# Optimization experiments

Hardware: AMD Instinct MI355X
Metric: run time of the kernel (lower is better)

## Reference

```python
import jax, jax.numpy as jnp
import numpy as np

# EISANI constants (inference path, dense non-EI weights, static connections)
NUM_BITS = 16        # EISANITABcontinuousVarEncodingNumBits
K_SYN = 32           # numberOfSynapsesPerSegment
SEGMENTS = 2         # numberOfSegmentsPerNeuron
THETA = 8            # segment activation threshold (synapse-count based)
H = 4096             # hiddenLayerSize
F = 128              # numberOfFeatures
C = 10               # numberOfClasses
B = 64               # batch


def _make_weight(key, h, s, p):
    """Dense weight [h, s, p] with exactly K_SYN nonzero +/-1 synapses per segment
    (mirrors _initialise_layer_weights dense non-EI branch)."""
    k1, k2 = jax.random.split(key)
    cols = jax.random.randint(k1, (h, s, K_SYN), 0, p)
    signs = jnp.where(jax.random.bernoulli(k2, 0.5, (h, s, K_SYN)), 1.0, -1.0).astype(jnp.float32)
    hh = jnp.arange(h)[:, None, None]
    ss = jnp.arange(s)[None, :, None]
    return jnp.zeros((h, s, p), jnp.float32).at[hh, ss, cols].set(signs)


def setup_inputs() -> dict:
    key = jax.random.key(0)
    kx, k0, k1, k2, ko = jax.random.split(key, 5)
    x = jax.random.uniform(kx, (B, F), dtype=jnp.float32)
    W0 = _make_weight(k0, H, SEGMENTS, F * NUM_BITS)
    W1 = _make_weight(k1, H, SEGMENTS, H)
    W2 = _make_weight(k2, H, SEGMENTS, H)
    outW = jax.random.normal(ko, (3, H, C), dtype=jnp.float32) * 0.02
    return {"x": x, "W0": W0, "W1": W1, "W2": W2, "outW": outW}


def _encode(x):
    # thermometer (graded) encoding of continuous vars into NUM_BITS binary bits
    thresholds = (jnp.arange(NUM_BITS, dtype=jnp.float32) + 1.0) / (NUM_BITS + 1.0)
    bits = (x[:, :, None] >= thresholds).astype(jnp.float32)  # [B, F, NUM_BITS]
    return bits.reshape(x.shape[0], -1)  # [B, F*NUM_BITS]


def reference(x, W0, W1, W2, outW):
    acts = _encode(x)  # [B, P0]
    layer_acts = []
    for W in (W0, W1, W2):
        # segment membrane sums over binary presynaptic activations
        z = jnp.einsum('bp,hsp->bhs', acts, W)  # [B, H, S]
        # neuron fires if ANY segment reaches threshold
        fired = jnp.any(z >= THETA, axis=-1)
        acts = fired.astype(jnp.float32)  # binary activation [B, H]
        layer_acts.append(acts)
    stacked = jnp.stack(layer_acts)  # [L, B, H]
    out = jnp.einsum('lbh,lhc->bc', stacked, outW)  # class scores [B, C]
    return out
```

## Files before the change

kernel.cpp:

```cpp
#include <hip/hip_runtime.h>
#include <hip/hip_bf16.h>

typedef unsigned long long u64;
typedef float f32x4 __attribute__((ext_vector_type(4)));

#define H_SZ 4096
#define NBITS 16
#define NFEAT 128
#define NCLS 10
#define THETA 8


__global__ void encode_kernel(const float* __restrict__ x, u64* __restrict__ actp0) {
    int idx = blockIdx.x * blockDim.x + threadIdx.x;
    if (idx >= 32 * 64) return;
    int wword = idx >> 6;
    int b = idx & 63;
    int c = wword >> 2, j = wword & 3;
    float thr0 = (4 * 0 + j + 1.0f) / (NBITS + 1.0f);
    float thr1 = (4 * 1 + j + 1.0f) / (NBITS + 1.0f);
    float thr2 = (4 * 2 + j + 1.0f) / (NBITS + 1.0f);
    float thr3 = (4 * 3 + j + 1.0f) / (NBITS + 1.0f);
    const float* xb = x + b * NFEAT + c * 16;
    u64 word = 0;
    #pragma unroll
    for (int k = 0; k < 16; k++) {
        float xv = xb[k];
        word |= (u64)(xv >= thr0) << (4 * k + 0);
        word |= (u64)(xv >= thr1) << (4 * k + 1);
        word |= (u64)(xv >= thr2) << (4 * k + 2);
        word |= (u64)(xv >= thr3) << (4 * k + 3);
    }
    actp0[wword * 64 + b] = word;
}

__device__ __forceinline__ u64 bfly_stage(u64 x, int lane, int d, u64 Md) {
    u64 p = __shfl_xor(x, d);
    return (lane & d) ? ((x & Md) | ((p >> d) & ~Md))
                      : ((x & ~Md) | ((p << d) & Md));
}

__device__ __forceinline__ u64 transpose64(u64 x, int lane) {
    x = bfly_stage(x, lane, 32, 0xFFFFFFFF00000000ULL);
    x = bfly_stage(x, lane, 16, 0xFFFF0000FFFF0000ULL);
    x = bfly_stage(x, lane,  8, 0xFF00FF00FF00FF00ULL);
    x = bfly_stage(x, lane,  4, 0xF0F0F0F0F0F0F0F0ULL);
    x = bfly_stage(x, lane,  2, 0xCCCCCCCCCCCCCCCCULL);
    x = bfly_stage(x, lane,  1, 0xAAAAAAAAAAAAAAAAULL);
    return x;
}

template <int P, bool FROM_FIRED>
__global__ __launch_bounds__(256, 4) void layer_kernel(const float* __restrict__ W,
                                                       const u64* __restrict__ actin,
                                                       u64* __restrict__ fired_out) {
    constexpr int NW = P / 64;
    constexpr int NC = P / 256;
    __shared__ __align__(16) u64 lds[NW * 64];
    int tid = threadIdx.x;
    int lane = tid & 63;
    int warp = tid >> 6;
    int h = blockIdx.x * 4 + warp;
    const f32x4* w0 = (const f32x4*)(W + (size_t)(2 * h) * P) + lane;
    const f32x4* w1 = (const f32x4*)(W + (size_t)(2 * h + 1) * P) + lane;

    f32x4 pa[4], pb[4];
    #pragma unroll
    for (int c = 0; c < 4; c++) {
        pa[c] = __builtin_nontemporal_load(w0 + c * 64);
        pb[c] = __builtin_nontemporal_load(w1 + c * 64);
    }

    if constexpr (FROM_FIRED) {
        #pragma unroll 4
        for (int c = 0; c < 16; c++) {
            u64 xw = actin[c * 256 + 4 * lane + warp];
            xw = transpose64(xw, lane);
            lds[(c * 4 + warp) * 64 + lane] = xw;
        }
    } else {
        const ulonglong2* src = (const ulonglong2*)actin;
        ulonglong2* dst = (ulonglong2*)lds;
        #pragma unroll
        for (int i = tid; i < NW * 32; i += 256) dst[i] = src[i];
    }
    __syncthreads();

    unsigned int zp0 = 0, zn0 = 0, zp1 = 0, zn1 = 0;
    auto body = [&](int c, f32x4 a, f32x4 b) {
        u64 A0 = lds[(c * 4 + 0) * 64 + lane];
        u64 A1 = lds[(c * 4 + 1) * 64 + lane];
        u64 A2 = lds[(c * 4 + 2) * 64 + lane];
        u64 A3 = lds[(c * 4 + 3) * 64 + lane];
        u64 m;
        m = __ballot(a.x > 0.0f); zp0 += __builtin_popcountll(A0 & m);
        m = __ballot(a.x < 0.0f); zn0 += __builtin_popcountll(A0 & m);
        m = __ballot(a.y > 0.0f); zp0 += __builtin_popcountll(A1 & m);
        m = __ballot(a.y < 0.0f); zn0 += __builtin_popcountll(A1 & m);
        m = __ballot(a.z > 0.0f); zp0 += __builtin_popcountll(A2 & m);
        m = __ballot(a.z < 0.0f); zn0 += __builtin_popcountll(A2 & m);
        m = __ballot(a.w > 0.0f); zp0 += __builtin_popcountll(A3 & m);
        m = __ballot(a.w < 0.0f); zn0 += __builtin_popcountll(A3 & m);

        m = __ballot(b.x > 0.0f); zp1 += __builtin_popcountll(A0 & m);
        m = __ballot(b.x < 0.0f); zn1 += __builtin_popcountll(A0 & m);
        m = __ballot(b.y > 0.0f); zp1 += __builtin_popcountll(A1 & m);
        m = __ballot(b.y < 0.0f); zn1 += __builtin_popcountll(A1 & m);
        m = __ballot(b.z > 0.0f); zp1 += __builtin_popcountll(A2 & m);
        m = __ballot(b.z < 0.0f); zn1 += __builtin_popcountll(A2 & m);
        m = __ballot(b.w > 0.0f); zp1 += __builtin_popcountll(A3 & m);
        m = __ballot(b.w < 0.0f); zn1 += __builtin_popcountll(A3 & m);
    };

    #pragma unroll
    for (int c = 0; c < 4; c++) body(c, pa[c], pb[c]);
    #pragma unroll 4
    for (int c = 4; c < NC; c++) {
        f32x4 a = __builtin_nontemporal_load(w0 + c * 64);
        f32x4 b = __builtin_nontemporal_load(w1 + c * 64);
        body(c, a, b);
    }

    int z0 = (int)zp0 - (int)zn0;
    int z1 = (int)zp1 - (int)zn1;
    u64 f0 = __ballot(z0 >= THETA);
    u64 f1 = __ballot(z1 >= THETA);
    if (lane == 0) fired_out[h] = f0 | f1;
}

__global__ void output_kernel(const float* __restrict__ outW,
                              const u64* __restrict__ fired,
                              float* __restrict__ out) {
    __shared__ float red[4][64];
    int tid = threadIdx.x;
    int lane = tid & 63;
    int warp = tid >> 6;
    int wid = blockIdx.x * 4 + warp;
    int l = wid / (NCLS * 64);
    int rem = wid % (NCLS * 64);
    int c = rem / 64;
    int chunk = rem % 64;
    const u64* fl = fired + l * H_SZ;
    int h0 = chunk * 64;
    float acc = 0.0f;
    #pragma unroll 8
    for (int h = h0; h < h0 + 64; h++) {
        float wv = outW[((size_t)(l * H_SZ + h)) * NCLS + c];
        if ((fl[h] >> lane) & 1ULL) acc += wv;
    }
    red[warp][lane] = acc;
    __syncthreads();
    if (warp == 0) {
        float s = red[0][lane] + red[1][lane] + red[2][lane] + red[3][lane];
        atomicAdd(&out[lane * NCLS + c], s);
    }
}

extern "C" void kernel_launch(void* const* d_in, const int* in_sizes, int n_in,
                              void* d_out, int out_size, void* d_ws, size_t ws_size,
                              hipStream_t stream) {
    const float* x    = (const float*)d_in[0];
    const float* W0   = (const float*)d_in[1];
    const float* W1   = (const float*)d_in[2];
    const float* W2   = (const float*)d_in[3];
    const float* outW = (const float*)d_in[4];
    float* out = (float*)d_out;

    char* ws = (char*)d_ws;
    u64* actp0 = (u64*)(ws);
    u64* fired = (u64*)(ws + 16384);

    hipMemsetAsync(d_out, 0, (size_t)out_size * sizeof(float), stream);

    encode_kernel<<<8, 256, 0, stream>>>(x, actp0);

    layer_kernel<2048, false><<<1024, 256, 0, stream>>>(W0, actp0, fired + 0 * H_SZ);
    layer_kernel<4096, true ><<<1024, 256, 0, stream>>>(W1, fired + 0 * H_SZ, fired + 1 * H_SZ);
    layer_kernel<4096, true ><<<1024, 256, 0, stream>>>(W2, fired + 1 * H_SZ, fired + 2 * H_SZ);

    output_kernel<<<480, 256, 0, stream>>>(outW, fired, out);
}
```

Baseline: 342.8 us.

## Assign one segment row per wavefront with 512-thread blocks; fold output memset into encode

Each layer block now uses 8 wavefronts, with each wave streaming a single segment row instead of both segments of one neuron. The two segment ballots are OR-combined through a small shared array after an extra barrier. This doubles the number of waves issuing weight loads, meant to raise memory-level parallelism on the bandwidth-bound dense weight stream, and halves the per-wave activation transpose work. Zeroing of the output is moved into the encode kernel so the separate memset launch goes away.

```diff
diff --git a/kernel.cpp b/kernel.cpp
--- a/kernel.cpp
+++ b/kernel.cpp
@@ -1,5 +1,4 @@
 #include <hip/hip_runtime.h>
-#include <hip/hip_bf16.h>
 
 typedef unsigned long long u64;
 typedef float f32x4 __attribute__((ext_vector_type(4)));
@@ -11,8 +10,11 @@
 #define THETA 8
 
 
-__global__ void encode_kernel(const float* __restrict__ x, u64* __restrict__ actp0) {
+__global__ void encode_kernel(const float* __restrict__ x, u64* __restrict__ actp0,
+                              float* __restrict__ out, int out_n) {
     int idx = blockIdx.x * blockDim.x + threadIdx.x;
+    if (blockIdx.x == 0)
+        for (int i = threadIdx.x; i < out_n; i += 256) out[i] = 0.0f;
     if (idx >= 32 * 64) return;
     int wword = idx >> 6;
     int b = idx & 63;
@@ -51,81 +53,64 @@
 }
 
 template <int P, bool FROM_FIRED>
-__global__ __launch_bounds__(256, 4) void layer_kernel(const float* __restrict__ W,
-                                                       const u64* __restrict__ actin,
-                                                       u64* __restrict__ fired_out) {
+__global__ __launch_bounds__(512, 8) void layer_kernel(
+    const float* __restrict__ W, const u64* __restrict__ actin,
+    u64* __restrict__ fired_out)
+{
+    constexpr int NC = P / 256;
     constexpr int NW = P / 64;
-    constexpr int NC = P / 256;
     __shared__ __align__(16) u64 lds[NW * 64];
+    __shared__ u64 bal[8];
     int tid = threadIdx.x;
     int lane = tid & 63;
     int warp = tid >> 6;
-    int h = blockIdx.x * 4 + warp;
-    const f32x4* w0 = (const f32x4*)(W + (size_t)(2 * h) * P) + lane;
-    const f32x4* w1 = (const f32x4*)(W + (size_t)(2 * h + 1) * P) + lane;
+    int row = blockIdx.x * 8 + warp;
+    const f32x4* wr = (const f32x4*)(W + (size_t)row * P) + lane;
 
-    f32x4 pa[4], pb[4];
+    f32x4 pw[4];
     #pragma unroll
-    for (int c = 0; c < 4; c++) {
-        pa[c] = __builtin_nontemporal_load(w0 + c * 64);
-        pb[c] = __builtin_nontemporal_load(w1 + c * 64);
-    }
+    for (int c = 0; c < 4; c++) pw[c] = __builtin_nontemporal_load(wr + c * 64);
 
     if constexpr (FROM_FIRED) {
-        #pragma unroll 4
-        for (int c = 0; c < 16; c++) {
-            u64 xw = actin[c * 256 + 4 * lane + warp];
+        #pragma unroll
+        for (int k = 0; k < 8; k++) {
+            int idx = warp * 8 + k;
+            u64 xw = actin[(idx >> 2) * 256 + 4 * lane + (idx & 3)];
             xw = transpose64(xw, lane);
-            lds[(c * 4 + warp) * 64 + lane] = xw;
+            lds[idx * 64 + lane] = xw;
         }
     } else {
         const ulonglong2* src = (const ulonglong2*)actin;
         ulonglong2* dst = (ulonglong2*)lds;
-        #pragma unroll
-        for (int i = tid; i < NW * 32; i += 256) dst[i] = src[i];
+        for (int i = tid; i < NW * 32; i += 512) dst[i] = src[i];
     }
     __syncthreads();
 
-    unsigned int zp0 = 0, zn0 = 0, zp1 = 0, zn1 = 0;
-    auto body = [&](int c, f32x4 a, f32x4 b) {
-        u64 A0 = lds[(c * 4 + 0) * 64 + lane];
-        u64 A1 = lds[(c * 4 + 1) * 64 + lane];
-        u64 A2 = lds[(c * 4 + 2) * 64 + lane];
-        u64 A3 = lds[(c * 4 + 3) * 64 + lane];
+    unsigned zp = 0, zn = 0;
+    auto body = [&](int c, f32x4 a) {
+        const u64* p = lds + c * 256 + lane;
+        u64 A0 = p[0], A1 = p[64], A2 = p[128], A3 = p[192];
         u64 m;
-        m = __ballot(a.x > 0.0f); zp0 += __builtin_popcountll(A0 & m);
-        m = __ballot(a.x < 0.0f); zn0 += __builtin_popcountll(A0 & m);
-        m = __ballot(a.y > 0.0f); zp0 += __builtin_popcountll(A1 & m);
-        m = __ballot(a.y < 0.0f); zn0 += __builtin_popcountll(A1 & m);
-        m = __ballot(a.z > 0.0f); zp0 += __builtin_popcountll(A2 & m);
-        m = __ballot(a.z < 0.0f); zn0 += __builtin_popcountll(A2 & m);
-        m = __ballot(a.w > 0.0f); zp0 += __builtin_popcountll(A3 & m);
-        m = __ballot(a.w < 0.0f); zn0 += __builtin_popcountll(A3 & m);
+        m = __ballot(a.x > 0.0f); zp += __builtin_popcountll(A0 & m);
+        m = __ballot(a.x < 0.0f); zn += __builtin_popcountll(A0 & m);
+        m = __ballot(a.y > 0.0f); zp += __builtin_popcountll(A1 & m);
+        m = __ballot(a.y < 0.0f); zn += __builtin_popcountll(A1 & m);
+        m = __ballot(a.z > 0.0f); zp += __builtin_popcountll(A2 & m);
+        m = __ballot(a.z < 0.0f); zn += __builtin_popcountll(A2 & m);
+        m = __ballot(a.w > 0.0f); zp += __builtin_popcountll(A3 & m);
+        m = __ballot(a.w < 0.0f); zn += __builtin_popcountll(A3 & m);
+    };
+    #pragma unroll
+    for (int c = 0; c < 4; c++) body(c, pw[c]);
+    #pragma unroll 4
+    for (int c = 4; c < NC; c++)
+        body(c, __builtin_nontemporal_load(wr + c * 64));
 
-        m = __ballot(b.x > 0.0f); zp1 += __builtin_popcountll(A0 & m);
-        m = __ballot(b.x < 0.0f); zn1 += __builtin_popcountll(A0 & m);
-        m = __ballot(b.y > 0.0f); zp1 += __builtin_popcountll(A1 & m);
-        m = __ballot(b.y < 0.0f); zn1 += __builtin_popcountll(A1 & m);
-        m = __ballot(b.z > 0.0f); zp1 += __builtin_popcountll(A2 & m);
-        m = __ballot(b.z < 0.0f); zn1 += __builtin_popcountll(A2 & m);
-        m = __ballot(b.w > 0.0f); zp1 += __builtin_popcountll(A3 & m);
-        m = __ballot(b.w < 0.0f); zn1 += __builtin_popcountll(A3 & m);
-    };
-
-    #pragma unroll
-    for (int c = 0; c < 4; c++) body(c, pa[c], pb[c]);
-    #pragma unroll 4
-    for (int c = 4; c < NC; c++) {
-        f32x4 a = __builtin_nontemporal_load(w0 + c * 64);
-        f32x4 b = __builtin_nontemporal_load(w1 + c * 64);
-        body(c, a, b);
-    }
-
-    int z0 = (int)zp0 - (int)zn0;
-    int z1 = (int)zp1 - (int)zn1;
-    u64 f0 = __ballot(z0 >= THETA);
-    u64 f1 = __ballot(z1 >= THETA);
-    if (lane == 0) fired_out[h] = f0 | f1;
+    int z = (int)zp - (int)zn;
+    u64 bz = __ballot(z >= THETA);
+    if (lane == 0) bal[warp] = bz;
+    __syncthreads();
+    if (tid < 4) fired_out[blockIdx.x * 4 + tid] = bal[2 * tid] | bal[2 * tid + 1];
 }
 
 __global__ void output_kernel(const float* __restrict__ outW,
@@ -167,16 +152,14 @@
     float* out = (float*)d_out;
 
     char* ws = (char*)d_ws;
-    u64* actp0 = (u64*)(ws);
-    u64* fired = (u64*)(ws + 16384);
+    u64* fired = (u64*)(ws);
+    u64* actp0 = (u64*)(ws + 98304);
 
-    hipMemsetAsync(d_out, 0, (size_t)out_size * sizeof(float), stream);
+    encode_kernel<<<8, 256, 0, stream>>>(x, actp0, out, out_size);
 
-    encode_kernel<<<8, 256, 0, stream>>>(x, actp0);
-
-    layer_kernel<2048, false><<<1024, 256, 0, stream>>>(W0, actp0, fired + 0 * H_SZ);
-    layer_kernel<4096, true ><<<1024, 256, 0, stream>>>(W1, fired + 0 * H_SZ, fired + 1 * H_SZ);
-    layer_kernel<4096, true ><<<1024, 256, 0, stream>>>(W2, fired + 1 * H_SZ, fired + 2 * H_SZ);
+    layer_kernel<2048, false><<<1024, 512, 0, stream>>>(W0, actp0, fired);
+    layer_kernel<4096, true ><<<1024, 512, 0, stream>>>(W1, fired, fired + H_SZ);
+    layer_kernel<4096, true ><<<1024, 512, 0, stream>>>(W2, fired + H_SZ, fired + 2 * H_SZ);
 
     output_kernel<<<480, 256, 0, stream>>>(outW, fired, out);
 }
```

Result: faster. 333.5 us (median of 2 runs) (-2.7%).
